# Performance work log

Measured on AMD Instinct MI355X. Metric: run time of the kernel, lower is better.

## Reference

```python
import jax, jax.numpy as jnp
import numpy as np

B, L, D_IN, H, N_BLOCKS, N_STATE, PRED = 2048, 168, 9, 96, 4, 96, 96
N2 = N_STATE // 2  # complex-conjugate pairs: keep half the state, double the real part


def s4d_kernel(log_dt, log_A_real, A_imag, C_re, C_im, length):
    # S4D (diagonal SSM) convolution kernel, ZOH-style discretization.
    dt = jnp.exp(log_dt)[:, None]                  # (H,1)
    A = -jnp.exp(log_A_real) + 1j * A_imag         # (H,N2)
    C = C_re + 1j * C_im                           # (H,N2)
    dtA = dt * A                                   # (H,N2)
    Ct = C * (jnp.exp(dtA) - 1.0) / A              # discretized C
    # Vandermonde: K[h,l] = 2*Re(sum_n Ct[h,n] * exp(dtA[h,n] * l))
    V = jnp.exp(dtA[:, :, None] * jnp.arange(length))  # (H,N2,L)
    return 2.0 * jnp.einsum('hn,hnl->hl', Ct, V).real  # (H,L)


def causal_conv(u, K):
    # u: (B,L,H), K: (H,L) -> causal depthwise convolution via FFT
    n = 2 * u.shape[1]
    Uf = jnp.fft.rfft(u, n=n, axis=1)              # (B,n/2+1,H)
    Kf = jnp.fft.rfft(K.T, n=n, axis=0)            # (n/2+1,H)
    return jnp.fft.irfft(Uf * Kf[None], n=n, axis=1)[:, :u.shape[1]]


def layer_norm(x, w, b):
    mu = x.mean(-1, keepdims=True)
    var = x.var(-1, keepdims=True)
    return (x - mu) / jnp.sqrt(var + 1e-5) * w + b


def setup_inputs() -> dict:
    key = jax.random.key(0)
    ks = jax.random.split(key, 20)
    r = lambda k, s, sc=1.0: jax.random.normal(k, s, jnp.float32) * sc
    inp = {
        'x': r(ks[0], (B, L, D_IN)),
        'enc_W': r(ks[1], (D_IN, H), 1.0 / np.sqrt(D_IN)),
        'enc_b': jnp.zeros((H,), jnp.float32),
        # per-block S4D parameters, stacked on leading n_blocks axis
        'log_dt': jax.random.uniform(ks[2], (N_BLOCKS, H), jnp.float32,
                                     np.log(1e-3), np.log(1e-1)),
        'log_A_real': jnp.full((N_BLOCKS, H, N2), np.log(0.5), jnp.float32),
        'A_imag': jnp.tile(np.pi * jnp.arange(N2, dtype=jnp.float32), (N_BLOCKS, H, 1)),
        'C_re': r(ks[3], (N_BLOCKS, H, N2), 0.5),
        'C_im': r(ks[4], (N_BLOCKS, H, N2), 0.5),
        'D_skip': r(ks[5], (N_BLOCKS, H)),
        'W_out': r(ks[6], (N_BLOCKS, H, H), 1.0 / np.sqrt(H)),
        'b_out': jnp.zeros((N_BLOCKS, H), jnp.float32),
        'ln_w': jnp.ones((N_BLOCKS, H), jnp.float32),
        'ln_b': jnp.zeros((N_BLOCKS, H), jnp.float32),
        'dec_W': r(ks[7], (H, H), 1.0 / np.sqrt(H)),
        'dec_b': jnp.zeros((H,), jnp.float32),
        'fc1_W': r(ks[8], (H * L, H), 1.0 / np.sqrt(H * L)),
        'fc1_b': jnp.zeros((H,), jnp.float32),
        'fc2_W': r(ks[9], (H, PRED), 1.0 / np.sqrt(H)),
        'fc2_b': jnp.zeros((PRED,), jnp.float32),
    }
    return inp


def reference(x, enc_W, enc_b, log_dt, log_A_real, A_imag, C_re, C_im, D_skip,
              W_out, b_out, ln_w, ln_b, dec_W, dec_b, fc1_W, fc1_b, fc2_W, fc2_b):
    h = x @ enc_W + enc_b                              # (B,L,H) encoder
    for i in range(N_BLOCKS):                          # post-norm residual S4 blocks
        K = s4d_kernel(log_dt[i], log_A_real[i], A_imag[i], C_re[i], C_im[i], L)
        z = causal_conv(h, K) + h * D_skip[i]          # SSM conv + skip D*u
        z = jax.nn.gelu(z)                             # activation (dropout off at eval)
        z = z @ W_out[i] + b_out[i]                    # output mixing
        h = layer_norm(h + z, ln_w[i], ln_b[i])        # residual + post-norm
    h = h @ dec_W + dec_b                              # S4Model decoder (d_model->d_model)
    out = h.reshape(h.shape[0], -1) @ fc1_W + fc1_b    # flatten + fc1
    out = out @ fc2_W + fc2_b                          # fc2 -> PRED_LEN
    return out[..., None]                              # (B,96,1)
```

## Files before the change

### kernel.cpp

```cpp
#include <hip/hip_runtime.h>
#include <hip/hip_bf16.h>
#include <math.h>

#define NB 4
#define B  2048
#define L  168
#define DI 9
#define H  96
#define N2 48

#define ZSTR2 132
#define CZ 68

typedef short short8 __attribute__((ext_vector_type(8)));
typedef float f32x4  __attribute__((ext_vector_type(4)));
typedef unsigned short u16x8 __attribute__((ext_vector_type(8)));
typedef unsigned short u16x4 __attribute__((ext_vector_type(4)));

__device__ __forceinline__ float gelu_f(float x) {
    float x2 = x * x;
    float e  = __builtin_amdgcn_exp2f(x * fmaf(0.1029432225f, x2, 2.3022081899f));
    float r  = __builtin_amdgcn_rcpf(e + 1.0f);
    return x * (1.0f - r);
}

__device__ __forceinline__ unsigned short bf16_rne(float x) {
    unsigned u = __float_as_uint(x);
    return (unsigned short)((u + 0x7FFFu + ((u >> 16) & 1u)) >> 16);
}
__device__ __forceinline__ float b2f(unsigned short v) {
    return __uint_as_float((unsigned)v << 16);
}

__global__ void kgen_kernel(const float* __restrict__ log_dt, const float* __restrict__ lar,
                            const float* __restrict__ aim, const float* __restrict__ cre,
                            const float* __restrict__ cim, float* __restrict__ K)
{
    const int ih   = blockIdx.x;
    const int lane = threadIdx.x;
    float ctre = 0.f, ctim = 0.f, pre = 0.f, pim = 0.f, mre = 0.f, mim = 0.f;
    if (lane < N2) {
        float dt  = expf(log_dt[ih]);
        int   idx = ih * N2 + lane;
        float reA = -expf(lar[idx]);
        float imA = aim[idx];
        float dre = dt * reA, dim = dt * imA;
        float er  = expf(dre);
        float sv, cv;
        sincosf(dim, &sv, &cv);
        mre = er * cv; mim = er * sv;
        float nre = mre - 1.0f, nim = mim;
        float den = reA * reA + imA * imA;
        float tre = (nre * reA + nim * imA) / den;
        float tim = (nim * reA - nre * imA) / den;
        float cr = cre[idx], ci = cim[idx];
        ctre = cr * tre - ci * tim;
        ctim = cr * tim + ci * tre;
        pre = 1.0f; pim = 0.0f;
    }
    float* Kr = K + ih * L;
    for (int l = 0; l < L; ++l) {
        float term = ctre * pre - ctim * pim;
        #pragma unroll
        for (int off = 32; off > 0; off >>= 1) term += __shfl_xor(term, off, 64);
        if (lane == 0) Kr[l] = 2.0f * term;
        float nr = pre * mre - pim * mim;
        float ni = pre * mim + pim * mre;
        pre = nr; pim = ni;
    }
}

__global__ void wprep_kernel(const float* __restrict__ wout, short* __restrict__ wfrag, int ntask)
{
    int idx = blockIdx.x * 256 + threadIdx.x;
    if (idx >= ntask) return;
    int layer = idx / 9216;  int rem  = idx - layer * 9216;
    int ch    = rem / 3072;  int rem2 = rem - ch * 3072;
    int m     = rem2 / 512;  int rem3 = rem2 - m * 512;
    int s     = rem3 / 256;  int rem4 = rem3 - s * 256;
    int lane  = rem4 / 4;    int d    = rem4 - lane * 4;
    int g = lane >> 4, c = lane & 15;
    int k  = ch * 32 + g * 8 + 2 * d;
    int hp = m * 16 + c;
    const float* Wl = wout + (size_t)layer * H * H;
    float w0 = Wl[k * H + hp];
    float w1 = Wl[(k + 1) * H + hp];
    unsigned short b0, b1;
    if (s == 0) { b0 = bf16_rne(w0); b1 = bf16_rne(w1); }
    else {
        unsigned short h0 = bf16_rne(w0), h1 = bf16_rne(w1);
        b0 = bf16_rne(w0 - b2f(h0));
        b1 = bf16_rne(w1 - b2f(h1));
    }
    wfrag[idx * 2]     = (short)b0;
    wfrag[idx * 2 + 1] = (short)b1;
}

__global__ void tgen_kernel(const float* __restrict__ Kg, short* __restrict__ tfrag)
{
    static const int kmaxA[11] = {0, 0, 1, 1, 2, 2, 3, 3, 4, 4, 5};
    static const int toffA[11] = {0, 1, 2, 4, 6, 9, 12, 16, 20, 25, 30};
    int idx = blockIdx.x * 256 + threadIdx.x;
    if (idx >= 96 * 66 * 64) return;
    int lane = idx & 63;
    int t    = (idx >> 6) % 66;
    int h    = (idx >> 6) / 66;
    int mi = t / 6, ki = t - mi * 6;
    if (ki > kmaxA[mi]) return;
    int g = lane >> 4, c = lane & 15;
    int row = mi * 16 + c;
    short8 a;
    #pragma unroll
    for (int j = 0; j < 8; ++j) {
        int kk = ki * 32 + g * 8 + j;
        int d  = row - kk;
        float val = (row < L && d >= 0) ? Kg[h * L + d] : 0.0f;
        a[j] = (short)bf16_rne(val);
    }
    short8* dst = (short8*)tfrag + (size_t)(h * 36 + toffA[mi] + ki) * 64;
    dst[lane] = a;
}

__launch_bounds__(256)
__global__ void wcomp_kernel(const float* __restrict__ decW, const float* __restrict__ decb,
                             const float* __restrict__ fc1W, float* __restrict__ wcs,
                             float* __restrict__ cbpart)
{
    __shared__ float Bs[96 * 100];
    const int tid = threadIdx.x;
    const int l   = blockIdx.x;
    for (int e = tid; e < 96 * 96; e += 256) {
        int h = e / 96, p = e - h * 96;
        Bs[h * 100 + p] = fc1W[(size_t)(l * 96 + h) * 96 + p];
    }
    __syncthreads();
    const int pt = tid & 31;
    const int kt = tid >> 5;
    float acc[12][3];
    #pragma unroll
    for (int kk = 0; kk < 12; ++kk)
        #pragma unroll
        for (int j = 0; j < 3; ++j) acc[kk][j] = 0.f;
    for (int h = 0; h < 96; ++h) {
        float dw[12];
        #pragma unroll
        for (int kk = 0; kk < 12; ++kk) dw[kk] = decW[(kt + 8 * kk) * 96 + h];
        float bs[3];
        #pragma unroll
        for (int j = 0; j < 3; ++j) bs[j] = Bs[h * 100 + pt + 32 * j];
        #pragma unroll
        for (int kk = 0; kk < 12; ++kk)
            #pragma unroll
            for (int j = 0; j < 3; ++j) acc[kk][j] = fmaf(dw[kk], bs[j], acc[kk][j]);
    }
    float* wl = wcs + (size_t)l * 9216;
    #pragma unroll
    for (int kk = 0; kk < 12; ++kk)
        #pragma unroll
        for (int j = 0; j < 3; ++j)
            wl[(kt + 8 * kk) * 96 + pt + 32 * j] = acc[kk][j];
    if (kt == 0) {
        #pragma unroll
        for (int j = 0; j < 3; ++j) {
            float s = 0.f;
            for (int h = 0; h < 96; ++h) s = fmaf(decb[h], Bs[h * 100 + pt + 32 * j], s);
            cbpart[l * 96 + pt + 32 * j] = s;
        }
    }
}

__global__ void cbias_red_kernel(const float* __restrict__ cbpart, const float* __restrict__ fc1b,
                                 float* __restrict__ cbias)
{
    int p = threadIdx.x;
    if (p < 96) {
        float s = fc1b[p];
        for (int l = 0; l < L; ++l) s += cbpart[l * 96 + p];
        cbias[p] = s;
    }
}

__launch_bounds__(256)
__global__ void enc2_kernel(const float* __restrict__ x, const float* __restrict__ W,
                            const float* __restrict__ bias, unsigned short* __restrict__ hb2)
{
    __shared__ float Ws[DI * H];
    __shared__ float bs[H];
    const int tid = threadIdx.x;
    const int l   = blockIdx.x;
    const int b0  = blockIdx.y * 256;
    for (int e = tid; e < DI * H; e += 256) Ws[e] = W[e];
    if (tid < H) bs[tid] = bias[tid];
    __syncthreads();
    float xv[DI];
    const float* xr = x + (size_t)(b0 + tid) * (L * DI) + l * DI;
    #pragma unroll
    for (int k = 0; k < DI; ++k) xv[k] = xr[k];
    for (int h = 0; h < H; ++h) {
        float a = bs[h];
        #pragma unroll
        for (int k = 0; k < DI; ++k) a = fmaf(xv[k], Ws[k * H + h], a);
        hb2[((size_t)h * L + l) * B + b0 + tid] = bf16_rne(a);
    }
}

__launch_bounds__(256, 4)
__global__ void conv3_kernel(const unsigned short* __restrict__ hb2, const short* __restrict__ tfrag,
                             const float* __restrict__ Dsk, unsigned short* __restrict__ z2)
{
    static const int toffA[11] = {0, 1, 2, 4, 6, 9, 12, 16, 20, 25, 30};
    __shared__ __align__(16) unsigned short zs[192 * CZ];
    const int tid  = threadIdx.x;
    const int w    = tid >> 6;
    const int lane = tid & 63;
    const int g    = lane >> 4;
    const int cc   = lane & 15;
    const int h    = blockIdx.x;
    const int b0   = blockIdx.y * 64;

    for (int e = tid; e < 168 * 8; e += 256) {
        int lp = e >> 3, b8 = e & 7;
        u16x8 v = *(const u16x8*)(hb2 + ((size_t)h * L + lp) * B + b0 + b8 * 8);
        *(u16x4*)(&zs[lp * CZ + b8 * 8])     = (u16x4){v[0], v[1], v[2], v[3]};
        *(u16x4*)(&zs[lp * CZ + b8 * 8 + 4]) = (u16x4){v[4], v[5], v[6], v[7]};
    }
    for (int e = tid; e < 24 * 8; e += 256) {
        int lp = 168 + (e >> 3), b8 = e & 7;
        *(u16x4*)(&zs[lp * CZ + b8 * 8])     = (u16x4){0, 0, 0, 0};
        *(u16x4*)(&zs[lp * CZ + b8 * 8 + 4]) = (u16x4){0, 0, 0, 0};
    }
    __syncthreads();

    f32x4 acc[11];
    #pragma unroll
    for (int mi = 0; mi < 11; ++mi) acc[mi] = (f32x4){0.f, 0.f, 0.f, 0.f};

    const int col = w * 16 + cc;
    const short8* Tbase = (const short8*)tfrag + (size_t)h * 36 * 64 + lane;

    #pragma unroll
    for (int ki = 0; ki < 6; ++ki) {
        short8 bh;
        #pragma unroll
        for (int j = 0; j < 8; ++j)
            bh[j] = (short)zs[(ki * 32 + g * 8 + j) * CZ + col];
        short8 tf[11];
        #pragma unroll
        for (int mi = 0; mi < 11; ++mi)
            if (mi >= 2 * ki)
                tf[mi] = Tbase[(size_t)(toffA[mi] + ki) * 64];
        #pragma unroll
        for (int mi = 0; mi < 11; ++mi)
            if (mi >= 2 * ki)
                acc[mi] = __builtin_amdgcn_mfma_f32_16x16x32_bf16(tf[mi], bh, acc[mi], 0, 0, 0);
    }

    const float ds = Dsk[h];
    #pragma unroll
    for (int mi = 0; mi < 11; ++mi) {
        #pragma unroll
        for (int r = 0; r < 4; ++r) {
            int l = mi * 16 + g * 4 + r;
            if (l < L) {
                float uu = b2f(zs[l * CZ + col]);
                float zv = gelu_f(fmaf(ds, uu, acc[mi][r]));
                zs[l * CZ + col] = bf16_rne(zv);
            }
        }
    }
    __syncthreads();
    for (int e = tid; e < 168 * 8; e += 256) {
        int lp = e >> 3, b8 = e & 7;
        u16x4 a = *(const u16x4*)(&zs[lp * CZ + b8 * 8]);
        u16x4 b = *(const u16x4*)(&zs[lp * CZ + b8 * 8 + 4]);
        u16x8 v = {a[0], a[1], a[2], a[3], b[0], b[1], b[2], b[3]};
        *(u16x8*)(z2 + ((size_t)h * L + lp) * B + b0 + b8 * 8) = v;
    }
}

__launch_bounds__(512)
__global__ void mix2_kernel(const unsigned short* __restrict__ z2, unsigned short* __restrict__ hb2,
                            const short* __restrict__ wfrag, const float* __restrict__ bout,
                            const float* __restrict__ lnw, const float* __restrict__ lnb)
{
    __shared__ __align__(16) unsigned short zs[H * ZSTR2];
    __shared__ __align__(16) unsigned short rs[H * ZSTR2];
    const int tid  = threadIdx.x;
    const int w    = tid >> 6;
    const int lane = tid & 63;
    const int g    = lane >> 4;
    const int cc   = lane & 15;
    const int l    = blockIdx.x;
    const int b0   = blockIdx.y * 128;

    for (int e = tid; e < 96 * 16; e += 512) {
        int hh = e >> 4, b8 = e & 15;
        u16x8 v = *(const u16x8*)(z2 + ((size_t)hh * L + l) * B + b0 + b8 * 8);
        *(u16x4*)(&zs[hh * ZSTR2 + b8 * 8])     = (u16x4){v[0], v[1], v[2], v[3]};
        *(u16x4*)(&zs[hh * ZSTR2 + b8 * 8 + 4]) = (u16x4){v[4], v[5], v[6], v[7]};
    }
    for (int e = tid; e < 96 * 16; e += 512) {
        int hh = e >> 4, b8 = e & 15;
        u16x8 v = *(const u16x8*)(hb2 + ((size_t)hh * L + l) * B + b0 + b8 * 8);
        *(u16x4*)(&rs[hh * ZSTR2 + b8 * 8])     = (u16x4){v[0], v[1], v[2], v[3]};
        *(u16x4*)(&rs[hh * ZSTR2 + b8 * 8 + 4]) = (u16x4){v[4], v[5], v[6], v[7]};
    }
    __syncthreads();

    f32x4 acc[6];
    #pragma unroll
    for (int m = 0; m < 6; ++m) acc[m] = (f32x4){0.f, 0.f, 0.f, 0.f};

    const int col = w * 16 + cc;

    #pragma unroll
    for (int ks = 0; ks < 3; ++ks) {
        short8 bh;
        #pragma unroll
        for (int j = 0; j < 8; ++j)
            bh[j] = (short)zs[(ks * 32 + g * 8 + j) * ZSTR2 + col];
        const short8* Wf = (const short8*)(wfrag) + ks * 12 * 64;
        short8 wa[12];
        #pragma unroll
        for (int m = 0; m < 12; ++m) wa[m] = Wf[m * 64 + lane];
        #pragma unroll
        for (int m = 0; m < 6; ++m) {
            acc[m] = __builtin_amdgcn_mfma_f32_16x16x32_bf16(wa[2 * m + 1], bh, acc[m], 0, 0, 0);
            acc[m] = __builtin_amdgcn_mfma_f32_16x16x32_bf16(wa[2 * m],     bh, acc[m], 0, 0, 0);
        }
    }

    float vals[6][4];
    float s = 0.f, q = 0.f;
    #pragma unroll
    for (int m = 0; m < 6; ++m) {
        float4 B4 = *(const float4*)(bout + m * 16 + g * 4);
        float bo[4] = {B4.x, B4.y, B4.z, B4.w};
        #pragma unroll
        for (int r = 0; r < 4; ++r) {
            int hr = m * 16 + g * 4 + r;
            float res = b2f(rs[hr * ZSTR2 + col]);
            float v = acc[m][r] + bo[r] + res;
            vals[m][r] = v;
            s += v; q += v * v;
        }
    }
    s += __shfl_xor(s, 16, 64); q += __shfl_xor(q, 16, 64);
    s += __shfl_xor(s, 32, 64); q += __shfl_xor(q, 32, 64);
    float mean = s * (1.0f / 96.0f);
    float var  = q * (1.0f / 96.0f) - mean * mean;
    float rstd = rsqrtf(var + 1e-5f);
    #pragma unroll
    for (int m = 0; m < 6; ++m) {
        float4 W4 = *(const float4*)(lnw + m * 16 + g * 4);
        float4 Bb = *(const float4*)(lnb + m * 16 + g * 4);
        float wv[4] = {W4.x, W4.y, W4.z, W4.w};
        float bv[4] = {Bb.x, Bb.y, Bb.z, Bb.w};
        #pragma unroll
        for (int r = 0; r < 4; ++r) {
            int hr = m * 16 + g * 4 + r;
            rs[hr * ZSTR2 + col] = bf16_rne(fmaf((vals[m][r] - mean) * rstd, wv[r], bv[r]));
        }
    }
    __syncthreads();
    for (int e = tid; e < 96 * 16; e += 512) {
        int hh = e >> 4, b8 = e & 15;
        u16x4 a = *(const u16x4*)(&rs[hh * ZSTR2 + b8 * 8]);
        u16x4 b = *(const u16x4*)(&rs[hh * ZSTR2 + b8 * 8 + 4]);
        u16x8 v = {a[0], a[1], a[2], a[3], b[0], b[1], b[2], b[3]};
        *(u16x8*)(hb2 + ((size_t)hh * L + l) * B + b0 + b8 * 8) = v;
    }
}

__launch_bounds__(256)
__global__ void fc1m_kernel(const unsigned short* __restrict__ hb2, const short* __restrict__ wcfrag,
                            float* __restrict__ partial)
{
    __shared__ __align__(16) unsigned short zs[H * ZSTR2];
    const int tid  = threadIdx.x;
    const int w    = tid >> 6;
    const int lane = tid & 63;
    const int g    = lane >> 4;
    const int cc   = lane & 15;
    const int ksp  = blockIdx.x;
    const int b0   = blockIdx.y * 128;

    f32x4 acc[2][6];
    #pragma unroll
    for (int n2 = 0; n2 < 2; ++n2)
        #pragma unroll
        for (int m = 0; m < 6; ++m) acc[n2][m] = (f32x4){0.f, 0.f, 0.f, 0.f};

    for (int il = 0; il < 4; ++il) {
        const int l = ksp * 4 + il;
        __syncthreads();
        for (int e = tid; e < 96 * 16; e += 256) {
            int hh = e >> 4, b8 = e & 15;
            u16x8 v = *(const u16x8*)(hb2 + ((size_t)hh * L + l) * B + b0 + b8 * 8);
            *(u16x4*)(&zs[hh * ZSTR2 + b8 * 8])     = (u16x4){v[0], v[1], v[2], v[3]};
            *(u16x4*)(&zs[hh * ZSTR2 + b8 * 8 + 4]) = (u16x4){v[4], v[5], v[6], v[7]};
        }
        __syncthreads();
        for (int ksl = 0; ksl < 3; ++ksl) {
            short8 bh[2];
            #pragma unroll
            for (int n2 = 0; n2 < 2; ++n2) {
                int col = (w * 2 + n2) * 16 + cc;
                #pragma unroll
                for (int j = 0; j < 8; ++j)
                    bh[n2][j] = (short)zs[(ksl * 32 + g * 8 + j) * ZSTR2 + col];
            }
            const short8* Wf = (const short8*)(wcfrag) + (size_t)(l * 3 + ksl) * 768;
            short8 wa[12];
            #pragma unroll
            for (int m = 0; m < 12; ++m) wa[m] = Wf[m * 64 + lane];
            #pragma unroll
            for (int m = 0; m < 6; ++m) {
                #pragma unroll
                for (int n2 = 0; n2 < 2; ++n2) {
                    acc[n2][m] = __builtin_amdgcn_mfma_f32_16x16x32_bf16(wa[2 * m + 1], bh[n2], acc[n2][m], 0, 0, 0);
                    acc[n2][m] = __builtin_amdgcn_mfma_f32_16x16x32_bf16(wa[2 * m],     bh[n2], acc[n2][m], 0, 0, 0);
                }
            }
        }
    }

    #pragma unroll
    for (int n2 = 0; n2 < 2; ++n2) {
        int gb = b0 + (w * 2 + n2) * 16 + cc;
        #pragma unroll
        for (int m = 0; m < 6; ++m) {
            *(float4*)&partial[((size_t)ksp * B + gb) * 96 + m * 16 + g * 4] =
                make_float4(acc[n2][m][0], acc[n2][m][1], acc[n2][m][2], acc[n2][m][3]);
        }
    }
}

__global__ void fc1red_kernel(const float* __restrict__ partial, const float* __restrict__ cbias,
                              float* __restrict__ t1)
{
    int o = blockIdx.x * 256 + threadIdx.x;
    int p = o % 96;
    float s = cbias[p];
    #pragma unroll 6
    for (int k = 0; k < 42; ++k) s += partial[(size_t)k * (B * 96) + o];
    t1[o] = s;
}

__launch_bounds__(256)
__global__ void fc2_kernel(const float* __restrict__ t1, const float* __restrict__ W,
                           const float* __restrict__ fb, float* __restrict__ out)
{
    __shared__ float Ws[96 * 100];
    const int tid = threadIdx.x;
    for (int e = tid; e < 96 * 96; e += 256) Ws[(e / 96) * 100 + (e % 96)] = W[e];
    __syncthreads();
    int o = blockIdx.x * 256 + tid;
    int b = o / 96, p = o - b * 96;
    const float* tr = t1 + b * 96;
    float acc = fb[p];
    #pragma unroll 4
    for (int h = 0; h < 96; ++h) acc = fmaf(tr[h], Ws[h * 100 + p], acc);
    out[o] = acc;
}

extern "C" void kernel_launch(void* const* d_in, const int* in_sizes, int n_in,
                              void* d_out, int out_size, void* d_ws, size_t ws_size,
                              hipStream_t stream)
{
    const float* x      = (const float*)d_in[0];
    const float* encW   = (const float*)d_in[1];
    const float* encb   = (const float*)d_in[2];
    const float* log_dt = (const float*)d_in[3];
    const float* lar    = (const float*)d_in[4];
    const float* aim    = (const float*)d_in[5];
    const float* cre    = (const float*)d_in[6];
    const float* cim    = (const float*)d_in[7];
    const float* dsk    = (const float*)d_in[8];
    const float* wout   = (const float*)d_in[9];
    const float* boutp  = (const float*)d_in[10];
    const float* lnw    = (const float*)d_in[11];
    const float* lnb    = (const float*)d_in[12];
    const float* decW   = (const float*)d_in[13];
    const float* decb   = (const float*)d_in[14];
    const float* fc1W   = (const float*)d_in[15];
    const float* fc1b   = (const float*)d_in[16];
    const float* fc2W   = (const float*)d_in[17];
    const float* fc2b   = (const float*)d_in[18];

    char*           ws      = (char*)d_ws;
    float*          K       = (float*)(ws);
    short*          wfrag   = (short*)(ws + ((size_t)384 << 10));
    float*          t1      = (float*)(ws + ((size_t)1 << 20));
    float*          cbpart  = (float*)(ws + ((size_t)1 << 20) + (900 << 10));
    float*          cbias   = (float*)(ws + ((size_t)1 << 20) + (980 << 10));
    short*          wcfrag  = (short*)(ws + ((size_t)2 << 20));
    short*          tfrag   = (short*)(ws + ((size_t)9 << 20));
    float*          wcs     = (float*)(ws + ((size_t)9 << 20));
    unsigned short* hb2     = (unsigned short*)(ws + ((size_t)16 << 20));
    unsigned short* z2      = (unsigned short*)(ws + ((size_t)80 << 20));
    float*          partial = (float*)(ws + ((size_t)80 << 20));

    kgen_kernel<<<NB * H, 64, 0, stream>>>(log_dt, lar, aim, cre, cim, K);
    wprep_kernel<<<144, 256, 0, stream>>>(wout, wfrag, NB * 9216);
    wcomp_kernel<<<L, 256, 0, stream>>>(decW, decb, fc1W, wcs, cbpart);
    wprep_kernel<<<6048, 256, 0, stream>>>(wcs, wcfrag, L * 9216);
    cbias_red_kernel<<<1, 128, 0, stream>>>(cbpart, fc1b, cbias);
    enc2_kernel<<<dim3(L, 8), 256, 0, stream>>>(x, encW, encb, hb2);
    for (int i = 0; i < NB; ++i) {
        tgen_kernel<<<1584, 256, 0, stream>>>(K + i * H * L, tfrag);
        conv3_kernel<<<dim3(H, 32), 256, 0, stream>>>(hb2, tfrag, dsk + i * H, z2);
        mix2_kernel<<<dim3(L, 16), 512, 0, stream>>>(z2, hb2, wfrag + i * 18432,
                                                     boutp + i * H, lnw + i * H, lnb + i * H);
    }
    fc1m_kernel<<<dim3(42, 16), 256, 0, stream>>>(hb2, wcfrag, partial);
    fc1red_kernel<<<768, 256, 0, stream>>>(partial, cbias, t1);
    fc2_kernel<<<768, 256, 0, stream>>>(t1, fc2W, fc2b, (float*)d_out);
}
```

Baseline: 526.6 us.

## Prefetch next sequence step into registers in mix2 and fc1m kernels

mix2 now handles two sequence positions per block, halving the grid. It loads the second position's z and residual tiles into registers while the first is computed. fc1m also prefetches the next l-slice into registers during the MFMA loop, then writes it to shared memory after a barrier. The aim is to hide global-load latency behind compute, at the cost of more registers, fewer blocks in mix2, and some extra barriers.

```diff
diff --git a/kernel.cpp b/kernel.cpp
--- a/kernel.cpp
+++ b/kernel.cpp
@@ -290,85 +290,112 @@
     const int lane = tid & 63;
     const int g    = lane >> 4;
     const int cc   = lane & 15;
-    const int l    = blockIdx.x;
+    const int l0   = blockIdx.x * 2;
     const int b0   = blockIdx.y * 128;
 
     for (int e = tid; e < 96 * 16; e += 512) {
         int hh = e >> 4, b8 = e & 15;
-        u16x8 v = *(const u16x8*)(z2 + ((size_t)hh * L + l) * B + b0 + b8 * 8);
+        u16x8 v = *(const u16x8*)(z2 + ((size_t)hh * L + l0) * B + b0 + b8 * 8);
         *(u16x4*)(&zs[hh * ZSTR2 + b8 * 8])     = (u16x4){v[0], v[1], v[2], v[3]};
         *(u16x4*)(&zs[hh * ZSTR2 + b8 * 8 + 4]) = (u16x4){v[4], v[5], v[6], v[7]};
     }
     for (int e = tid; e < 96 * 16; e += 512) {
         int hh = e >> 4, b8 = e & 15;
-        u16x8 v = *(const u16x8*)(hb2 + ((size_t)hh * L + l) * B + b0 + b8 * 8);
+        u16x8 v = *(const u16x8*)(hb2 + ((size_t)hh * L + l0) * B + b0 + b8 * 8);
         *(u16x4*)(&rs[hh * ZSTR2 + b8 * 8])     = (u16x4){v[0], v[1], v[2], v[3]};
         *(u16x4*)(&rs[hh * ZSTR2 + b8 * 8 + 4]) = (u16x4){v[4], v[5], v[6], v[7]};
     }
     __syncthreads();
 
-    f32x4 acc[6];
-    #pragma unroll
-    for (int m = 0; m < 6; ++m) acc[m] = (f32x4){0.f, 0.f, 0.f, 0.f};
-
     const int col = w * 16 + cc;
-
-    #pragma unroll
-    for (int ks = 0; ks < 3; ++ks) {
-        short8 bh;
-        #pragma unroll
-        for (int j = 0; j < 8; ++j)
-            bh[j] = (short)zs[(ks * 32 + g * 8 + j) * ZSTR2 + col];
-        const short8* Wf = (const short8*)(wfrag) + ks * 12 * 64;
-        short8 wa[12];
-        #pragma unroll
-        for (int m = 0; m < 12; ++m) wa[m] = Wf[m * 64 + lane];
+    u16x8 zr[3], rr[3];
+
+    for (int half = 0; half < 2; ++half) {
+        const int l = l0 + half;
+        if (half == 0) {
+            #pragma unroll
+            for (int i = 0; i < 3; ++i) {
+                int e = tid + i * 512;
+                int hh = e >> 4, b8 = e & 15;
+                zr[i] = *(const u16x8*)(z2 + ((size_t)hh * L + l0 + 1) * B + b0 + b8 * 8);
+                rr[i] = *(const u16x8*)(hb2 + ((size_t)hh * L + l0 + 1) * B + b0 + b8 * 8);
+            }
+        }
+
+        f32x4 acc[6];
+        #pragma unroll
+        for (int m = 0; m < 6; ++m) acc[m] = (f32x4){0.f, 0.f, 0.f, 0.f};
+
+        #pragma unroll
+        for (int ks = 0; ks < 3; ++ks) {
+            short8 bh;
+            #pragma unroll
+            for (int j = 0; j < 8; ++j)
+                bh[j] = (short)zs[(ks * 32 + g * 8 + j) * ZSTR2 + col];
+            const short8* Wf = (const short8*)(wfrag) + ks * 12 * 64;
+            short8 wa[12];
+            #pragma unroll
+            for (int m = 0; m < 12; ++m) wa[m] = Wf[m * 64 + lane];
+            #pragma unroll
+            for (int m = 0; m < 6; ++m) {
+                acc[m] = __builtin_amdgcn_mfma_f32_16x16x32_bf16(wa[2 * m + 1], bh, acc[m], 0, 0, 0);
+                acc[m] = __builtin_amdgcn_mfma_f32_16x16x32_bf16(wa[2 * m],     bh, acc[m], 0, 0, 0);
+            }
+        }
+
+        float vals[6][4];
+        float s = 0.f, q = 0.f;
         #pragma unroll
         for (int m = 0; m < 6; ++m) {
-            acc[m] = __builtin_amdgcn_mfma_f32_16x16x32_bf16(wa[2 * m + 1], bh, acc[m], 0, 0, 0);
-            acc[m] = __builtin_amdgcn_mfma_f32_16x16x32_bf16(wa[2 * m],     bh, acc[m], 0, 0, 0);
-        }
-    }
-
-    float vals[6][4];
-    float s = 0.f, q = 0.f;
-    #pragma unroll
-    for (int m = 0; m < 6; ++m) {
-        float4 B4 = *(const float4*)(bout + m * 16 + g * 4);
-        float bo[4] = {B4.x, B4.y, B4.z, B4.w};
-        #pragma unroll
-        for (int r = 0; r < 4; ++r) {
-            int hr = m * 16 + g * 4 + r;
-            float res = b2f(rs[hr * ZSTR2 + col]);
-            float v = acc[m][r] + bo[r] + res;
-            vals[m][r] = v;
-            s += v; q += v * v;
-        }
-    }
-    s += __shfl_xor(s, 16, 64); q += __shfl_xor(q, 16, 64);
-    s += __shfl_xor(s, 32, 64); q += __shfl_xor(q, 32, 64);
-    float mean = s * (1.0f / 96.0f);
-    float var  = q * (1.0f / 96.0f) - mean * mean;
-    float rstd = rsqrtf(var + 1e-5f);
-    #pragma unroll
-    for (int m = 0; m < 6; ++m) {
-        float4 W4 = *(const float4*)(lnw + m * 16 + g * 4);
-        float4 Bb = *(const float4*)(lnb + m * 16 + g * 4);
-        float wv[4] = {W4.x, W4.y, W4.z, W4.w};
-        float bv[4] = {Bb.x, Bb.y, Bb.z, Bb.w};
-        #pragma unroll
-        for (int r = 0; r < 4; ++r) {
-            int hr = m * 16 + g * 4 + r;
-            rs[hr * ZSTR2 + col] = bf16_rne(fmaf((vals[m][r] - mean) * rstd, wv[r], bv[r]));
-        }
-    }
-    __syncthreads();
-    for (int e = tid; e < 96 * 16; e += 512) {
-        int hh = e >> 4, b8 = e & 15;
-        u16x4 a = *(const u16x4*)(&rs[hh * ZSTR2 + b8 * 8]);
-        u16x4 b = *(const u16x4*)(&rs[hh * ZSTR2 + b8 * 8 + 4]);
-        u16x8 v = {a[0], a[1], a[2], a[3], b[0], b[1], b[2], b[3]};
-        *(u16x8*)(hb2 + ((size_t)hh * L + l) * B + b0 + b8 * 8) = v;
+            float4 B4 = *(const float4*)(bout + m * 16 + g * 4);
+            float bo[4] = {B4.x, B4.y, B4.z, B4.w};
+            #pragma unroll
+            for (int r = 0; r < 4; ++r) {
+                int hr = m * 16 + g * 4 + r;
+                float res = b2f(rs[hr * ZSTR2 + col]);
+                float v = acc[m][r] + bo[r] + res;
+                vals[m][r] = v;
+                s += v; q += v * v;
+            }
+        }
+        s += __shfl_xor(s, 16, 64); q += __shfl_xor(q, 16, 64);
+        s += __shfl_xor(s, 32, 64); q += __shfl_xor(q, 32, 64);
+        float mean = s * (1.0f / 96.0f);
+        float var  = q * (1.0f / 96.0f) - mean * mean;
+        float rstd = rsqrtf(var + 1e-5f);
+        #pragma unroll
+        for (int m = 0; m < 6; ++m) {
+            float4 W4 = *(const float4*)(lnw + m * 16 + g * 4);
+            float4 Bb = *(const float4*)(lnb + m * 16 + g * 4);
+            float wv[4] = {W4.x, W4.y, W4.z, W4.w};
+            float bv[4] = {Bb.x, Bb.y, Bb.z, Bb.w};
+            #pragma unroll
+            for (int r = 0; r < 4; ++r) {
+                int hr = m * 16 + g * 4 + r;
+                rs[hr * ZSTR2 + col] = bf16_rne(fmaf((vals[m][r] - mean) * rstd, wv[r], bv[r]));
+            }
+        }
+        __syncthreads();
+        for (int e = tid; e < 96 * 16; e += 512) {
+            int hh = e >> 4, b8 = e & 15;
+            u16x4 a = *(const u16x4*)(&rs[hh * ZSTR2 + b8 * 8]);
+            u16x4 b = *(const u16x4*)(&rs[hh * ZSTR2 + b8 * 8 + 4]);
+            u16x8 v = {a[0], a[1], a[2], a[3], b[0], b[1], b[2], b[3]};
+            *(u16x8*)(hb2 + ((size_t)hh * L + l) * B + b0 + b8 * 8) = v;
+        }
+        if (half == 0) {
+            __syncthreads();
+            #pragma unroll
+            for (int i = 0; i < 3; ++i) {
+                int e = tid + i * 512;
+                int hh = e >> 4, b8 = e & 15;
+                *(u16x4*)(&zs[hh * ZSTR2 + b8 * 8])     = (u16x4){zr[i][0], zr[i][1], zr[i][2], zr[i][3]};
+                *(u16x4*)(&zs[hh * ZSTR2 + b8 * 8 + 4]) = (u16x4){zr[i][4], zr[i][5], zr[i][6], zr[i][7]};
+                *(u16x4*)(&rs[hh * ZSTR2 + b8 * 8])     = (u16x4){rr[i][0], rr[i][1], rr[i][2], rr[i][3]};
+                *(u16x4*)(&rs[hh * ZSTR2 + b8 * 8 + 4]) = (u16x4){rr[i][4], rr[i][5], rr[i][6], rr[i][7]};
+            }
+            __syncthreads();
+        }
     }
 }
 
@@ -391,16 +418,25 @@
         #pragma unroll
         for (int m = 0; m < 6; ++m) acc[n2][m] = (f32x4){0.f, 0.f, 0.f, 0.f};
 
+    for (int e = tid; e < 96 * 16; e += 256) {
+        int hh = e >> 4, b8 = e & 15;
+        u16x8 v = *(const u16x8*)(hb2 + ((size_t)hh * L + ksp * 4) * B + b0 + b8 * 8);
+        *(u16x4*)(&zs[hh * ZSTR2 + b8 * 8])     = (u16x4){v[0], v[1], v[2], v[3]};
+        *(u16x4*)(&zs[hh * ZSTR2 + b8 * 8 + 4]) = (u16x4){v[4], v[5], v[6], v[7]};
+    }
+    __syncthreads();
+
+    u16x8 pr[6];
     for (int il = 0; il < 4; ++il) {
         const int l = ksp * 4 + il;
-        __syncthreads();
-        for (int e = tid; e < 96 * 16; e += 256) {
-            int hh = e >> 4, b8 = e & 15;
-            u16x8 v = *(const u16x8*)(hb2 + ((size_t)hh * L + l) * B + b0 + b8 * 8);
-            *(u16x4*)(&zs[hh * ZSTR2 + b8 * 8])     = (u16x4){v[0], v[1], v[2], v[3]};
-            *(u16x4*)(&zs[hh * ZSTR2 + b8 * 8 + 4]) = (u16x4){v[4], v[5], v[6], v[7]};
-        }
-        __syncthreads();
+        if (il < 3) {
+            #pragma unroll
+            for (int i = 0; i < 6; ++i) {
+                int e = tid + i * 256;
+                int hh = e >> 4, b8 = e & 15;
+                pr[i] = *(const u16x8*)(hb2 + ((size_t)hh * L + l + 1) * B + b0 + b8 * 8);
+            }
+        }
         for (int ksl = 0; ksl < 3; ++ksl) {
             short8 bh[2];
             #pragma unroll
@@ -422,6 +458,17 @@
                     acc[n2][m] = __builtin_amdgcn_mfma_f32_16x16x32_bf16(wa[2 * m],     bh[n2], acc[n2][m], 0, 0, 0);
                 }
             }
+        }
+        __syncthreads();
+        if (il < 3) {
+            #pragma unroll
+            for (int i = 0; i < 6; ++i) {
+                int e = tid + i * 256;
+                int hh = e >> 4, b8 = e & 15;
+                *(u16x4*)(&zs[hh * ZSTR2 + b8 * 8])     = (u16x4){pr[i][0], pr[i][1], pr[i][2], pr[i][3]};
+                *(u16x4*)(&zs[hh * ZSTR2 + b8 * 8 + 4]) = (u16x4){pr[i][4], pr[i][5], pr[i][6], pr[i][7]};
+            }
+            __syncthreads();
         }
     }
 
@@ -510,8 +557,8 @@
     for (int i = 0; i < NB; ++i) {
         tgen_kernel<<<1584, 256, 0, stream>>>(K + i * H * L, tfrag);
         conv3_kernel<<<dim3(H, 32), 256, 0, stream>>>(hb2, tfrag, dsk + i * H, z2);
-        mix2_kernel<<<dim3(L, 16), 512, 0, stream>>>(z2, hb2, wfrag + i * 18432,
-                                                     boutp + i * H, lnw + i * H, lnb + i * H);
+        mix2_kernel<<<dim3(L / 2, 16), 512, 0, stream>>>(z2, hb2, wfrag + i * 18432,
+                                                         boutp + i * H, lnw + i * H, lnb + i * H);
     }
     fc1m_kernel<<<dim3(42, 16), 256, 0, stream>>>(hb2, wcfrag, partial);
     fc1red_kernel<<<768, 256, 0, stream>>>(partial, cbias, t1);
```

Result: slower. 618.2 us (+17.4%).
